# Performance work log

Measured on AMD Instinct MI355X. Metric: run time of the kernel, lower is better.

The kernel has to match this reference:

```python
import jax, jax.numpy as jnp
import numpy as np

NUM_HEADS = 8
LN_EPS = 1e-5

def _ln(x, g, b):
    mu = jnp.mean(x, axis=-1, keepdims=True)
    var = jnp.mean((x - mu) ** 2, axis=-1, keepdims=True)
    return (x - mu) * jax.lax.rsqrt(var + LN_EPS) * g + b

def _rel_index(H, W):
    coords = np.stack(np.meshgrid(np.arange(H), np.arange(W), indexing='ij'))  # (2,H,W)
    cf = coords.reshape(2, -1)
    rel = (cf[:, :, None] - cf[:, None, :]).transpose(1, 2, 0)  # (N,N,2)
    rel = rel + np.array([H - 1, W - 1])
    rel[..., 0] *= 2 * W - 1
    return rel.sum(-1)  # (N,N) int

def _biases(H, W):
    bh = np.arange(1 - H, H)
    bw = np.arange(1 - W, W)
    b = np.stack(np.meshgrid(bh, bw, indexing='ij')).reshape(2, -1).T
    return b.astype(np.float32)  # ((2H-1)*(2W-1), 2)

def setup_inputs() -> dict:
    key = jax.random.key(0)
    ks = jax.random.split(key, 8)
    dim, heads, pd = 256, NUM_HEADS, 16
    B, H, W = 256, 16, 16
    s = lambda k, shp, fan: jax.random.normal(k, shp, jnp.float32) * (fan ** -0.5)
    return {
        'x': jax.random.normal(ks[0], (B, dim, H, W), jnp.float32),
        'qkv_w': s(ks[1], (3 * dim, dim), dim), 'qkv_b': jnp.zeros((3 * dim,), jnp.float32),
        'proj_w': s(ks[2], (dim, dim), dim), 'proj_b': jnp.zeros((dim,), jnp.float32),
        'pos_proj_w': s(ks[3], (pd, 2), 2), 'pos_proj_b': jnp.zeros((pd,), jnp.float32),
        'ln1_g': jnp.ones((pd,), jnp.float32), 'ln1_b': jnp.zeros((pd,), jnp.float32),
        'fc1_w': s(ks[4], (pd, pd), pd), 'fc1_b': jnp.zeros((pd,), jnp.float32),
        'ln2_g': jnp.ones((pd,), jnp.float32), 'ln2_b': jnp.zeros((pd,), jnp.float32),
        'fc2_w': s(ks[5], (pd, pd), pd), 'fc2_b': jnp.zeros((pd,), jnp.float32),
        'ln3_g': jnp.ones((pd,), jnp.float32), 'ln3_b': jnp.zeros((pd,), jnp.float32),
        'fc3_w': s(ks[6], (heads, pd), pd), 'fc3_b': jnp.zeros((heads,), jnp.float32),
    }

def reference(x, qkv_w, qkv_b, proj_w, proj_b, pos_proj_w, pos_proj_b,
              ln1_g, ln1_b, fc1_w, fc1_b, ln2_g, ln2_b, fc2_w, fc2_b,
              ln3_g, ln3_b, fc3_w, fc3_b):
    B, C, H, W = x.shape
    N, h = H * W, NUM_HEADS
    d = C // h
    scale = d ** -0.5
    xt = x.reshape(B, C, N).transpose(0, 2, 1)  # (B,N,C)
    qkv = (jnp.einsum('bnc,oc->bno', xt, qkv_w) + qkv_b)
    qkv = qkv.reshape(B, N, 3, h, d).transpose(2, 0, 3, 1, 4)  # (3,B,h,N,d)
    q, k, v = qkv[0] * scale, qkv[1], qkv[2]
    attn = jnp.einsum('bhnd,bhmd->bhnm', q, k)  # (B,h,N,N)
    # dynamic position bias MLP over ((2H-1)(2W-1), 2) offsets
    biases = jnp.asarray(_biases(H, W))
    p = biases @ pos_proj_w.T + pos_proj_b
    p = jax.nn.relu(_ln(p, ln1_g, ln1_b)) @ fc1_w.T + fc1_b
    p = jax.nn.relu(_ln(p, ln2_g, ln2_b)) @ fc2_w.T + fc2_b
    p = jax.nn.relu(_ln(p, ln3_g, ln3_b)) @ fc3_w.T + fc3_b  # (L, h)
    idx = jnp.asarray(_rel_index(H, W))  # (N,N)
    rpb = p[idx].transpose(2, 0, 1)  # (h,N,N)
    attn = jax.nn.softmax(attn + rpb[None], axis=-1)
    out = jnp.einsum('bhnm,bhmd->bhnd', attn, v).transpose(0, 2, 1, 3).reshape(B, N, C)
    out = jnp.einsum('bnc,oc->bno', out, proj_w) + proj_b
    return out.transpose(0, 2, 1).reshape(B, C, H, W)
```

## Files before the change

kernel.cpp:

```cpp
#include <hip/hip_runtime.h>

typedef __bf16 bf16;
typedef __bf16 bf16x8 __attribute__((ext_vector_type(8)));
typedef __bf16 bf16x4 __attribute__((ext_vector_type(4)));
typedef float f32x4 __attribute__((ext_vector_type(4)));
typedef float f32x16 __attribute__((ext_vector_type(16)));
typedef unsigned int u32;
typedef unsigned int u32x2 __attribute__((ext_vector_type(2)));
typedef unsigned int u32x4 __attribute__((ext_vector_type(4)));

#define MFMA16(a, b, c) __builtin_amdgcn_mfma_f32_16x16x32_bf16(a, b, c, 0, 0, 0)
#define MFMA32(a, b, c) __builtin_amdgcn_mfma_f32_32x32x16_bf16(a, b, c, 0, 0, 0)

__device__ __forceinline__ u32 pack2(float a, float b) {
  unsigned short ua = __builtin_bit_cast(unsigned short, (bf16)a);
  unsigned short ub = __builtin_bit_cast(unsigned short, (bf16)b);
  return (u32)ua | ((u32)ub << 16);
}

__device__ __forceinline__ void lnrelu16(const float* in, float* out,
                                         const float* __restrict__ g,
                                         const float* __restrict__ b) {
  float mu = 0.f;
#pragma unroll
  for (int t = 0; t < 16; ++t) mu += in[t];
  mu *= 0.0625f;
  float var = 0.f;
#pragma unroll
  for (int t = 0; t < 16; ++t) { float d = in[t] - mu; var += d * d; }
  var *= 0.0625f;
  float inv = rsqrtf(var + 1e-5f);
#pragma unroll
  for (int t = 0; t < 16; ++t) {
    float v = (in[t] - mu) * inv * g[t] + b[t];
    out[t] = fmaxf(v, 0.f);
  }
}

__global__ __launch_bounds__(256) void k_prep(
    const float* __restrict__ qkvw, bf16* __restrict__ wqkv,
    const float* __restrict__ pjw, bf16* __restrict__ wpj,
    const float* __restrict__ ppw, const float* __restrict__ ppb,
    const float* __restrict__ g1, const float* __restrict__ b1,
    const float* __restrict__ f1w, const float* __restrict__ f1b,
    const float* __restrict__ g2, const float* __restrict__ b2,
    const float* __restrict__ f2w, const float* __restrict__ f2b,
    const float* __restrict__ g3, const float* __restrict__ b3,
    const float* __restrict__ f3w, const float* __restrict__ f3b,
    float* __restrict__ ptab) {
  const int blk = blockIdx.x;
  if (blk < 96) {
    int t = blk * 256 + threadIdx.x;
    int lane = t & 63, fk = t >> 6;
    int ot = fk >> 3, kc = fk & 7;
    int o = ot * 16 + (lane & 15), cb = kc * 32 + (lane >> 4) * 8;
    const float* src = qkvw + o * 256 + cb;
    bf16x8 v;
#pragma unroll
    for (int j = 0; j < 8; ++j) v[j] = (bf16)src[j];
    *(bf16x8*)(wqkv + (size_t)t * 8) = v;
  } else if (blk < 160) {
    int i = (blk - 96) * 256 + threadIdx.x;
    if (i < 16384) {
      float4 v = ((const float4*)pjw)[i];
      bf16x4 o;
      o[0] = (bf16)v.x; o[1] = (bf16)v.y; o[2] = (bf16)v.z; o[3] = (bf16)v.w;
      ((bf16x4*)wpj)[i] = o;
    }
  } else {
    int l = (blk - 160) * 256 + threadIdx.x;
    if (l >= 961) return;
    float dh = (float)(l / 31) - 15.f;
    float dw = (float)(l % 31) - 15.f;
    float p[16], a[16], y[16];
#pragma unroll
    for (int t = 0; t < 16; ++t)
      p[t] = dh * ppw[2 * t] + dw * ppw[2 * t + 1] + ppb[t];
    lnrelu16(p, a, g1, b1);
#pragma unroll
    for (int t = 0; t < 16; ++t) {
      float s = f1b[t];
#pragma unroll
      for (int u = 0; u < 16; ++u) s += a[u] * f1w[t * 16 + u];
      y[t] = s;
    }
    lnrelu16(y, a, g2, b2);
#pragma unroll
    for (int t = 0; t < 16; ++t) {
      float s = f2b[t];
#pragma unroll
      for (int u = 0; u < 16; ++u) s += a[u] * f2w[t * 16 + u];
      p[t] = s;
    }
    lnrelu16(p, a, g3, b3);
#pragma unroll
    for (int t = 0; t < 8; ++t) {
      float s = f3b[t];
#pragma unroll
      for (int u = 0; u < 16; ++u) s += a[u] * f3w[t * 16 + u];
      ptab[l * 8 + t] = s;
    }
  }
}

__global__ __launch_bounds__(256) void k_bias(const float* __restrict__ ptab,
                                              bf16* __restrict__ Bsw) {
  int idx = blockIdx.x * 256 + threadIdx.x;
  int lane = idx & 63, tg = idx >> 6;
  int h = tg >> 6, qt = (tg >> 3) & 7, kt2 = tg & 7;
  int l31 = lane & 31, hi2 = lane >> 5;
  int n = qt * 32 + l31;
  int i1 = n >> 4, j1 = n & 15;
  bf16x8 o0, o1;
#pragma unroll
  for (int reg = 0; reg < 16; ++reg) {
    int key = kt2 * 32 + (reg & 3) + 8 * (reg >> 2) + 4 * hi2;
    int i2 = key >> 4, j2 = key & 15;
    int li = (i1 - i2 + 15) * 31 + (j1 - j2 + 15);
    bf16 v = (bf16)ptab[li * 8 + h];
    if (reg < 8) o0[reg] = v; else o1[reg - 8] = v;
  }
  bf16* dst = Bsw + tg * 1024 + lane * 16;
  *(bf16x8*)dst = o0;
  *(bf16x8*)(dst + 8) = o1;
}

__global__ __launch_bounds__(256) void k_qkv(
    const float* __restrict__ x, const bf16* __restrict__ Wf,
    const float* __restrict__ qb, bf16* __restrict__ q, bf16* __restrict__ kk,
    bf16* __restrict__ vT) {
  __shared__ bf16 Xl[64 * 256];
  __shared__ bf16 Vb[4][16 * 36];
  const int b = blockIdx.x >> 2;
  const int n_base = (blockIdx.x & 3) * 64;
  const int tid = threadIdx.x;
  const int lane = tid & 63;
  const int wo = tid >> 6;
  const int l15 = lane & 15, l4 = lane >> 4;

  {
    const float* xb = x + b * 65536 + n_base;
    const int p = tid & 3;
    const int Q = tid >> 2;
    const int nq = (Q & 15) * 4;
    const int cg = Q >> 4;
#pragma unroll
    for (int it = 0; it < 16; ++it) {
      const int c0 = (cg + it * 4) * 4;
      float4 v = *(const float4*)(xb + (c0 + p) * 256 + nq);
      u32 u0 = pack2(v.x, v.y);
      u32 u1 = pack2(v.z, v.w);
      u32 su0 = __shfl_xor(u0, 1);
      u32 su1 = __shfl_xor(u1, 1);
      u32 w, z;
      if (p & 1) {
        w = (su0 >> 16) | (u0 & 0xffff0000u);
        z = (su1 >> 16) | (u1 & 0xffff0000u);
      } else {
        w = (u0 & 0xffffu) | (su0 << 16);
        z = (u1 & 0xffffu) | (su1 << 16);
      }
      u32 sw = __shfl_xor(w, 2);
      u32 sz = __shfl_xor(z, 2);
      u32x2 o2;
      o2[0] = (p & 2) ? sz : w;
      o2[1] = (p & 2) ? z : sw;
      const int n = nq + p;
      const int wb = (2 * c0) ^ ((n & 7) << 4);
      *(u32x2*)((char*)Xl + n * 512 + wb) = o2;
    }
  }
  __syncthreads();

  const f32x4 fz = {0.f, 0.f, 0.f, 0.f};
  bf16* lb = Vb[wo];
  for (int og = 0; og < 3; ++og) {
    const int ot0 = wo * 12 + og * 4;
    f32x4 acc[4][4];
#pragma unroll
    for (int nt = 0; nt < 4; ++nt)
#pragma unroll
      for (int oi = 0; oi < 4; ++oi) acc[nt][oi] = fz;
#pragma unroll
    for (int kc = 0; kc < 8; ++kc) {
      bf16x8 afr[4], bfr[4];
#pragma unroll
      for (int nt = 0; nt < 4; ++nt) {
        int nn = nt * 16 + l15;
        int wb = (kc * 64 + l4 * 16) ^ ((nn & 7) << 4);
        afr[nt] = *(const bf16x8*)((const char*)Xl + nn * 512 + wb);
      }
#pragma unroll
      for (int oi = 0; oi < 4; ++oi)
        bfr[oi] = *(const bf16x8*)(Wf + ((((ot0 + oi) * 8) + kc) * 64 + lane) * 8);
#pragma unroll
      for (int nt = 0; nt < 4; ++nt)
#pragma unroll
        for (int oi = 0; oi < 4; ++oi)
          acc[nt][oi] = MFMA16(afr[nt], bfr[oi], acc[nt][oi]);
    }
#pragma unroll
    for (int oi = 0; oi < 4; ++oi) {
      int ot = ot0 + oi;
      int o = ot * 16 + l15;
      float bias = qb[o];
      int seg = o >> 8;
      int h = (o >> 5) & 7;
      int d = o & 31;
      int base = (b * 8 + h) * 8192;
#pragma unroll
      for (int pr = 0; pr < 2; ++pr) {
        f32x4 acc0 = acc[2 * pr][oi], acc1 = acc[2 * pr + 1][oi];
        int n0p = n_base + pr * 32;
        if (seg == 0) {
          bf16* dq = q + base + d;
#pragma unroll
          for (int nt = 0; nt < 2; ++nt)
#pragma unroll
            for (int r = 0; r < 4; ++r) {
              int n = n0p + nt * 16 + l4 * 4 + r;
              float v = nt ? acc1[r] : acc0[r];
              dq[n * 32] = (bf16)((v + bias) * 0.17677669529663687f);
            }
        } else if (seg == 1) {
          bf16* dk = kk + base + d;
#pragma unroll
          for (int nt = 0; nt < 2; ++nt)
#pragma unroll
            for (int r = 0; r < 4; ++r) {
              int n = n0p + nt * 16 + l4 * 4 + r;
              float v = nt ? acc1[r] : acc0[r];
              dk[n * 32] = (bf16)(v + bias);
            }
        } else {
#pragma unroll
          for (int nt = 0; nt < 2; ++nt) {
            f32x4 a = nt ? acc1 : acc0;
            *(u32*)(lb + l15 * 36 + nt * 16 + l4 * 4) =
                pack2(a[0] + bias, a[1] + bias);
            *(u32*)(lb + l15 * 36 + nt * 16 + l4 * 4 + 2) =
                pack2(a[2] + bias, a[3] + bias);
          }
          asm volatile("s_waitcnt lgkmcnt(0)" ::: "memory");
          __builtin_amdgcn_sched_barrier(0);
          int dl = lane >> 2, chv = lane & 3;
          bf16x4 rv0 = *(bf16x4*)(lb + dl * 36 + chv * 8);
          bf16x4 rv1 = *(bf16x4*)(lb + dl * 36 + chv * 8 + 4);
          asm volatile("s_waitcnt lgkmcnt(0)" ::: "memory");
          __builtin_amdgcn_sched_barrier(0);
          int d2 = (ot & 1) * 16 + dl;
          bf16* dv2 = vT + base + d2 * 256 + n0p + chv * 8;
          *(bf16x4*)dv2 = rv0;
          *(bf16x4*)(dv2 + 4) = rv1;
        }
      }
    }
  }
}

__global__ __launch_bounds__(256, 4) void k_attn(
    const bf16* __restrict__ q, const bf16* __restrict__ kk,
    const bf16* __restrict__ vT, const bf16* __restrict__ Bsw,
    bf16* __restrict__ ao) {
  __shared__ bf16 Kl[256 * 36];
  __shared__ bf16 Ob[4][32 * 36];
  const int bh = blockIdx.x;
  const int b = bh >> 3, h = bh & 7;
  const int tid = threadIdx.x;
  const int lane = tid & 63, wave = tid >> 6;
  const int l31 = lane & 31, hi = lane >> 5;

  const bf16* Kg = kk + bh * 8192;
#pragma unroll
  for (int i = 0; i < 4; ++i) {
    int t = tid + i * 256;
    int n = t >> 2, dc = t & 3;
    *(bf16x8*)(Kl + n * 36 + dc * 8) = *(const bf16x8*)(Kg + n * 32 + dc * 8);
  }
  __syncthreads();

  const bf16* Vg = vT + bh * 8192;
  bf16* ob = Ob[wave];
  for (int qi = 0; qi < 2; ++qi) {
    const int qt = wave * 2 + qi, q0 = qt * 32;
    bf16x8 qf0 = *(const bf16x8*)(q + bh * 8192 + (q0 + l31) * 32 + hi * 8);
    bf16x8 qf1 = *(const bf16x8*)(q + bh * 8192 + (q0 + l31) * 32 + 16 + hi * 8);
    const bf16* bq = Bsw + (h * 8 + qt) * 8192 + lane * 16;
    float lsum = 0.f;
    f32x16 o;
#pragma unroll
    for (int i = 0; i < 16; ++i) o[i] = 0.f;
#pragma unroll
    for (int kt2 = 0; kt2 < 8; ++kt2) {
      u32x4 w0 = *(const u32x4*)(bq + kt2 * 1024);
      u32x4 w1 = *(const u32x4*)(bq + kt2 * 1024 + 8);
      f32x16 acc;
#pragma unroll
      for (int j = 0; j < 4; ++j) {
        acc[2 * j] = __builtin_bit_cast(float, w0[j] << 16);
        acc[2 * j + 1] = __builtin_bit_cast(float, w0[j] & 0xffff0000u);
        acc[8 + 2 * j] = __builtin_bit_cast(float, w1[j] << 16);
        acc[8 + 2 * j + 1] = __builtin_bit_cast(float, w1[j] & 0xffff0000u);
      }
      bf16x8 kf0 = *(const bf16x8*)(Kl + (kt2 * 32 + l31) * 36 + hi * 8);
      bf16x8 kf1 = *(const bf16x8*)(Kl + (kt2 * 32 + l31) * 36 + 16 + hi * 8);
      acc = MFMA32(kf0, qf0, acc);
      acc = MFMA32(kf1, qf1, acc);
      u32 lo[4], hw[4];
#pragma unroll
      for (int qq = 0; qq < 4; ++qq) {
        float e0 = __expf(acc[4 * qq]);
        float e1 = __expf(acc[4 * qq + 1]);
        float e2 = __expf(acc[4 * qq + 2]);
        float e3 = __expf(acc[4 * qq + 3]);
        lsum += (e0 + e1) + (e2 + e3);
        lo[qq] = pack2(e0, e1);
        hw[qq] = pack2(e2, e3);
      }
#pragma unroll
      for (int sb = 0; sb < 2; ++sb) {
        u32 keep_lo = hi ? lo[2 * sb + 1] : lo[2 * sb];
        u32 keep_hi = hi ? hw[2 * sb + 1] : hw[2 * sb];
        u32 send_lo = hi ? lo[2 * sb] : lo[2 * sb + 1];
        u32 send_hi = hi ? hw[2 * sb] : hw[2 * sb + 1];
        u32 rlo = __shfl_xor(send_lo, 32);
        u32 rhi = __shfl_xor(send_hi, 32);
        u32x4 bw;
        bw[0] = hi ? rlo : keep_lo;
        bw[1] = hi ? rhi : keep_hi;
        bw[2] = hi ? keep_lo : rlo;
        bw[3] = hi ? keep_hi : rhi;
        bf16x8 pf = __builtin_bit_cast(bf16x8, bw);
        bf16x8 vf = *(const bf16x8*)(Vg + l31 * 256 + kt2 * 32 + sb * 16 + hi * 8);
        o = MFMA32(vf, pf, o);
      }
    }
    lsum += __shfl_xor(lsum, 32);
    const float inv = 1.f / lsum;
#pragma unroll
    for (int qq = 0; qq < 4; ++qq) {
      *(u32*)(ob + l31 * 36 + 8 * qq + 4 * hi) =
          pack2(o[4 * qq] * inv, o[4 * qq + 1] * inv);
      *(u32*)(ob + l31 * 36 + 8 * qq + 4 * hi + 2) =
          pack2(o[4 * qq + 2] * inv, o[4 * qq + 3] * inv);
    }
    asm volatile("s_waitcnt lgkmcnt(0)" ::: "memory");
    __builtin_amdgcn_sched_barrier(0);
    int n2 = lane >> 1, ch = lane & 1;
    bf16x4 r0 = *(bf16x4*)(ob + n2 * 36 + ch * 16);
    bf16x4 r1 = *(bf16x4*)(ob + n2 * 36 + ch * 16 + 4);
    bf16x4 r2 = *(bf16x4*)(ob + n2 * 36 + ch * 16 + 8);
    bf16x4 r3 = *(bf16x4*)(ob + n2 * 36 + ch * 16 + 12);
    asm volatile("s_waitcnt lgkmcnt(0)" ::: "memory");
    __builtin_amdgcn_sched_barrier(0);
    bf16* dst = ao + (b * 256 + q0 + n2) * 256 + h * 32 + ch * 16;
    *(bf16x4*)dst = r0;
    *(bf16x4*)(dst + 4) = r1;
    *(bf16x4*)(dst + 8) = r2;
    *(bf16x4*)(dst + 12) = r3;
  }
}

__global__ __launch_bounds__(512) void k_proj(
    const bf16* __restrict__ ao, const bf16* __restrict__ Wp,
    const float* __restrict__ pb, float* __restrict__ out) {
  __shared__ bf16 Sl[2][16 * 264];
  const int b = blockIdx.x & 255;
  const int oh = blockIdx.x >> 8;
  const int tid = threadIdx.x;
  const int lane = tid & 63, wave = tid >> 6;
  const int l15 = lane & 15, l4 = lane >> 4;
  const int ot = oh * 8 + wave;
  bf16x8 af[8];
  const bf16* wr = Wp + (ot * 16 + l15) * 256 + l4 * 8;
#pragma unroll
  for (int kc = 0; kc < 8; ++kc) af[kc] = *(const bf16x8*)(wr + kc * 32);
  float bias[4];
#pragma unroll
  for (int r = 0; r < 4; ++r) bias[r] = pb[ot * 16 + l4 * 4 + r];
  const bf16* aob = ao + b * 65536;
  float* outb = out + b * 65536 + ot * 16 * 256;
  const int sr = tid >> 5, sc = (tid & 31) * 8;

  *(bf16x8*)(Sl[0] + sr * 264 + sc) = *(const bf16x8*)(aob + sr * 256 + sc);
  __syncthreads();

  const f32x4 fz = {0.f, 0.f, 0.f, 0.f};
  for (int nt = 0; nt < 16; ++nt) {
    const int cur = nt & 1;
    if (nt < 15)
      *(bf16x8*)(Sl[cur ^ 1] + sr * 264 + sc) =
          *(const bf16x8*)(aob + ((nt + 1) * 16 + sr) * 256 + sc);
    f32x4 acc = fz;
#pragma unroll
    for (int kc = 0; kc < 8; ++kc) {
      bf16x8 bfr = *(const bf16x8*)(Sl[cur] + l15 * 264 + kc * 32 + l4 * 8);
      acc = MFMA16(af[kc], bfr, acc);
    }
#pragma unroll
    for (int r = 0; r < 4; ++r)
      outb[(l4 * 4 + r) * 256 + nt * 16 + l15] = acc[r] + bias[r];
    __syncthreads();
  }
}

extern "C" void kernel_launch(void* const* d_in, const int* in_sizes, int n_in,
                              void* d_out, int out_size, void* d_ws, size_t ws_size,
                              hipStream_t stream) {
  const float* x    = (const float*)d_in[0];
  const float* qkvw = (const float*)d_in[1];
  const float* qkvb = (const float*)d_in[2];
  const float* pjw  = (const float*)d_in[3];
  const float* pjb  = (const float*)d_in[4];
  const float* ppw  = (const float*)d_in[5];
  const float* ppb  = (const float*)d_in[6];
  const float* g1 = (const float*)d_in[7];   const float* b1 = (const float*)d_in[8];
  const float* f1w = (const float*)d_in[9];  const float* f1b = (const float*)d_in[10];
  const float* g2 = (const float*)d_in[11];  const float* b2 = (const float*)d_in[12];
  const float* f2w = (const float*)d_in[13]; const float* f2b = (const float*)d_in[14];
  const float* g3 = (const float*)d_in[15];  const float* b3 = (const float*)d_in[16];
  const float* f3w = (const float*)d_in[17]; const float* f3b = (const float*)d_in[18];
  float* out = (float*)d_out;

  bf16* wsq  = (bf16*)d_ws;
  bf16* wsk  = wsq + 16777216;
  bf16* wsv  = wsk + 16777216;
  bf16* wsao = wsv + 16777216;
  float* ptab = (float*)(wsao + 16777216);
  bf16* wqkv = (bf16*)(ptab + 8192);
  bf16* wpj  = wqkv + 196608;
  bf16* bsw  = wpj + 65536;

  hipLaunchKernelGGL(k_prep, dim3(164), dim3(256), 0, stream, qkvw, wqkv, pjw,
                     wpj, ppw, ppb, g1, b1, f1w, f1b, g2, b2, f2w, f2b, g3, b3,
                     f3w, f3b, ptab);
  hipLaunchKernelGGL(k_bias, dim3(128), dim3(256), 0, stream, ptab, bsw);
  hipLaunchKernelGGL(k_qkv, dim3(1024), dim3(256), 0, stream, x, wqkv, qkvb,
                     wsq, wsk, wsv);
  hipLaunchKernelGGL(k_attn, dim3(2048), dim3(256), 0, stream, wsq, wsk, wsv,
                     bsw, wsao);
  hipLaunchKernelGGL(k_proj, dim3(512), dim3(512), 0, stream, wsao, wpj, pjb, out);
}
```

Baseline: 160.6 us.

## Fuse QKV projection into per-(batch, head) attention kernel via LDS

The separate QKV GEMM kernel and attention kernel are merged into one kernel. Each (batch, head) block projects its own q, k and v into LDS from a double-buffered bf16 staging of x, then runs the attention loop on that LDS data. The weight prep is reordered so each head's slice is contiguous. This removes the global write and re-read of the q, k and vT intermediates and one launch. In exchange, each batch's input x is re-read and re-converted once per head. The kernel also uses about 77 KB of LDS with a lower occupancy bound.

```diff
diff --git a/kernel.cpp b/kernel.cpp
--- a/kernel.cpp
+++ b/kernel.cpp
@@ -37,8 +37,38 @@
   }
 }
 
+__device__ __forceinline__ void stage_slice(const float* __restrict__ xb,
+                                            int kc, bf16* dst, int tid) {
+  const int p = tid & 3;
+  const int Q = tid >> 2;
+  const int n0 = Q * 4;
+#pragma unroll
+  for (int it = 0; it < 8; ++it) {
+    const int c0 = it * 4;
+    float4 v = *(const float4*)(xb + (kc * 32 + c0 + p) * 256 + n0);
+    u32 u0 = pack2(v.x, v.y);
+    u32 u1 = pack2(v.z, v.w);
+    u32 su0 = __shfl_xor(u0, 1);
+    u32 su1 = __shfl_xor(u1, 1);
+    u32 w, z;
+    if (p & 1) {
+      w = (su0 >> 16) | (u0 & 0xffff0000u);
+      z = (su1 >> 16) | (u1 & 0xffff0000u);
+    } else {
+      w = (u0 & 0xffffu) | (su0 << 16);
+      z = (u1 & 0xffffu) | (su1 << 16);
+    }
+    u32 sw = __shfl_xor(w, 2);
+    u32 sz = __shfl_xor(z, 2);
+    u32x2 o2;
+    o2[0] = (p & 2) ? sz : w;
+    o2[1] = (p & 2) ? z : sw;
+    *(u32x2*)((char*)dst + (n0 + p) * 80 + 2 * c0) = o2;
+  }
+}
+
 __global__ __launch_bounds__(256) void k_prep(
-    const float* __restrict__ qkvw, bf16* __restrict__ wqkv,
+    const float* __restrict__ qkvw, bf16* __restrict__ whf,
     const float* __restrict__ pjw, bf16* __restrict__ wpj,
     const float* __restrict__ ppw, const float* __restrict__ ppb,
     const float* __restrict__ g1, const float* __restrict__ b1,
@@ -52,13 +82,16 @@
   if (blk < 96) {
     int t = blk * 256 + threadIdx.x;
     int lane = t & 63, fk = t >> 6;
-    int ot = fk >> 3, kc = fk & 7;
-    int o = ot * 16 + (lane & 15), cb = kc * 32 + (lane >> 4) * 8;
+    int kc = fk & 7, ht = fk >> 3;
+    int h = ht / 6, tt = ht % 6;
+    int seg = tt >> 1, dh = tt & 1;
+    int o = seg * 256 + h * 32 + dh * 16 + (lane & 15);
+    int cb = kc * 32 + (lane >> 4) * 8;
     const float* src = qkvw + o * 256 + cb;
     bf16x8 v;
 #pragma unroll
     for (int j = 0; j < 8; ++j) v[j] = (bf16)src[j];
-    *(bf16x8*)(wqkv + (size_t)t * 8) = v;
+    *(bf16x8*)(whf + (size_t)t * 8) = v;
   } else if (blk < 160) {
     int i = (blk - 96) * 256 + threadIdx.x;
     if (i < 16384) {
@@ -125,166 +158,96 @@
   *(bf16x8*)(dst + 8) = o1;
 }
 
-__global__ __launch_bounds__(256) void k_qkv(
-    const float* __restrict__ x, const bf16* __restrict__ Wf,
-    const float* __restrict__ qb, bf16* __restrict__ q, bf16* __restrict__ kk,
-    bf16* __restrict__ vT) {
-  __shared__ bf16 Xl[64 * 256];
-  __shared__ bf16 Vb[4][16 * 36];
-  const int b = blockIdx.x >> 2;
-  const int n_base = (blockIdx.x & 3) * 64;
-  const int tid = threadIdx.x;
-  const int lane = tid & 63;
-  const int wo = tid >> 6;
-  const int l15 = lane & 15, l4 = lane >> 4;
-
-  {
-    const float* xb = x + b * 65536 + n_base;
-    const int p = tid & 3;
-    const int Q = tid >> 2;
-    const int nq = (Q & 15) * 4;
-    const int cg = Q >> 4;
-#pragma unroll
-    for (int it = 0; it < 16; ++it) {
-      const int c0 = (cg + it * 4) * 4;
-      float4 v = *(const float4*)(xb + (c0 + p) * 256 + nq);
-      u32 u0 = pack2(v.x, v.y);
-      u32 u1 = pack2(v.z, v.w);
-      u32 su0 = __shfl_xor(u0, 1);
-      u32 su1 = __shfl_xor(u1, 1);
-      u32 w, z;
-      if (p & 1) {
-        w = (su0 >> 16) | (u0 & 0xffff0000u);
-        z = (su1 >> 16) | (u1 & 0xffff0000u);
-      } else {
-        w = (u0 & 0xffffu) | (su0 << 16);
-        z = (u1 & 0xffffu) | (su1 << 16);
-      }
-      u32 sw = __shfl_xor(w, 2);
-      u32 sz = __shfl_xor(z, 2);
-      u32x2 o2;
-      o2[0] = (p & 2) ? sz : w;
-      o2[1] = (p & 2) ? z : sw;
-      const int n = nq + p;
-      const int wb = (2 * c0) ^ ((n & 7) << 4);
-      *(u32x2*)((char*)Xl + n * 512 + wb) = o2;
-    }
-  }
-  __syncthreads();
-
-  const f32x4 fz = {0.f, 0.f, 0.f, 0.f};
-  bf16* lb = Vb[wo];
-  for (int og = 0; og < 3; ++og) {
-    const int ot0 = wo * 12 + og * 4;
-    f32x4 acc[4][4];
-#pragma unroll
-    for (int nt = 0; nt < 4; ++nt)
-#pragma unroll
-      for (int oi = 0; oi < 4; ++oi) acc[nt][oi] = fz;
-#pragma unroll
-    for (int kc = 0; kc < 8; ++kc) {
-      bf16x8 afr[4], bfr[4];
-#pragma unroll
-      for (int nt = 0; nt < 4; ++nt) {
-        int nn = nt * 16 + l15;
-        int wb = (kc * 64 + l4 * 16) ^ ((nn & 7) << 4);
-        afr[nt] = *(const bf16x8*)((const char*)Xl + nn * 512 + wb);
-      }
-#pragma unroll
-      for (int oi = 0; oi < 4; ++oi)
-        bfr[oi] = *(const bf16x8*)(Wf + ((((ot0 + oi) * 8) + kc) * 64 + lane) * 8);
-#pragma unroll
-      for (int nt = 0; nt < 4; ++nt)
-#pragma unroll
-        for (int oi = 0; oi < 4; ++oi)
-          acc[nt][oi] = MFMA16(afr[nt], bfr[oi], acc[nt][oi]);
-    }
-#pragma unroll
-    for (int oi = 0; oi < 4; ++oi) {
-      int ot = ot0 + oi;
-      int o = ot * 16 + l15;
-      float bias = qb[o];
-      int seg = o >> 8;
-      int h = (o >> 5) & 7;
-      int d = o & 31;
-      int base = (b * 8 + h) * 8192;
-#pragma unroll
-      for (int pr = 0; pr < 2; ++pr) {
-        f32x4 acc0 = acc[2 * pr][oi], acc1 = acc[2 * pr + 1][oi];
-        int n0p = n_base + pr * 32;
-        if (seg == 0) {
-          bf16* dq = q + base + d;
-#pragma unroll
-          for (int nt = 0; nt < 2; ++nt)
-#pragma unroll
-            for (int r = 0; r < 4; ++r) {
-              int n = n0p + nt * 16 + l4 * 4 + r;
-              float v = nt ? acc1[r] : acc0[r];
-              dq[n * 32] = (bf16)((v + bias) * 0.17677669529663687f);
-            }
-        } else if (seg == 1) {
-          bf16* dk = kk + base + d;
-#pragma unroll
-          for (int nt = 0; nt < 2; ++nt)
-#pragma unroll
-            for (int r = 0; r < 4; ++r) {
-              int n = n0p + nt * 16 + l4 * 4 + r;
-              float v = nt ? acc1[r] : acc0[r];
-              dk[n * 32] = (bf16)(v + bias);
-            }
-        } else {
-#pragma unroll
-          for (int nt = 0; nt < 2; ++nt) {
-            f32x4 a = nt ? acc1 : acc0;
-            *(u32*)(lb + l15 * 36 + nt * 16 + l4 * 4) =
-                pack2(a[0] + bias, a[1] + bias);
-            *(u32*)(lb + l15 * 36 + nt * 16 + l4 * 4 + 2) =
-                pack2(a[2] + bias, a[3] + bias);
-          }
-          asm volatile("s_waitcnt lgkmcnt(0)" ::: "memory");
-          __builtin_amdgcn_sched_barrier(0);
-          int dl = lane >> 2, chv = lane & 3;
-          bf16x4 rv0 = *(bf16x4*)(lb + dl * 36 + chv * 8);
-          bf16x4 rv1 = *(bf16x4*)(lb + dl * 36 + chv * 8 + 4);
-          asm volatile("s_waitcnt lgkmcnt(0)" ::: "memory");
-          __builtin_amdgcn_sched_barrier(0);
-          int d2 = (ot & 1) * 16 + dl;
-          bf16* dv2 = vT + base + d2 * 256 + n0p + chv * 8;
-          *(bf16x4*)dv2 = rv0;
-          *(bf16x4*)(dv2 + 4) = rv1;
-        }
-      }
-    }
-  }
-}
-
-__global__ __launch_bounds__(256, 4) void k_attn(
-    const bf16* __restrict__ q, const bf16* __restrict__ kk,
-    const bf16* __restrict__ vT, const bf16* __restrict__ Bsw,
+__global__ __launch_bounds__(256, 2) void k_fused(
+    const float* __restrict__ x, const bf16* __restrict__ Whf,
+    const float* __restrict__ qb, const bf16* __restrict__ Bsw,
     bf16* __restrict__ ao) {
-  __shared__ bf16 Kl[256 * 36];
-  __shared__ bf16 Ob[4][32 * 36];
-  const int bh = blockIdx.x;
-  const int b = bh >> 3, h = bh & 7;
+  __shared__ bf16 lds[38400];
+  bf16* Xs0 = lds;
+  bf16* Xs1 = lds + 10240;
+  bf16* qL  = lds;
+  bf16* kL  = lds + 20480;
+  bf16* vTL = lds + 29696;
+  const int b = blockIdx.x & 255;
+  const int h = blockIdx.x >> 8;
   const int tid = threadIdx.x;
   const int lane = tid & 63, wave = tid >> 6;
+  const int l15 = lane & 15, l4 = lane >> 4;
   const int l31 = lane & 31, hi = lane >> 5;
-
-  const bf16* Kg = kk + bh * 8192;
-#pragma unroll
-  for (int i = 0; i < 4; ++i) {
-    int t = tid + i * 256;
-    int n = t >> 2, dc = t & 3;
-    *(bf16x8*)(Kl + n * 36 + dc * 8) = *(const bf16x8*)(Kg + n * 32 + dc * 8);
-  }
+  const int w64 = wave * 64;
+  const float* xb = x + b * 65536;
+
+  const f32x4 fz = {0.f, 0.f, 0.f, 0.f};
+  f32x4 acc[4][6];
+#pragma unroll
+  for (int nt = 0; nt < 4; ++nt)
+#pragma unroll
+    for (int t = 0; t < 6; ++t) acc[nt][t] = fz;
+
+  stage_slice(xb, 0, Xs0, tid);
   __syncthreads();
-
-  const bf16* Vg = vT + bh * 8192;
-  bf16* ob = Ob[wave];
+#pragma unroll
+  for (int kc = 0; kc < 8; ++kc) {
+    if (kc < 7) stage_slice(xb, kc + 1, (kc & 1) ? Xs0 : Xs1, tid);
+    const bf16* Xc = (kc & 1) ? Xs1 : Xs0;
+    bf16x8 afr[4], bfr[6];
+#pragma unroll
+    for (int nt = 0; nt < 4; ++nt)
+      afr[nt] = *(const bf16x8*)((const char*)Xc + (w64 + nt * 16 + l15) * 80 +
+                                 l4 * 16);
+#pragma unroll
+    for (int t = 0; t < 6; ++t)
+      bfr[t] = *(const bf16x8*)(Whf + (((h * 6 + t) * 8 + kc) * 64 + lane) * 8);
+#pragma unroll
+    for (int nt = 0; nt < 4; ++nt)
+#pragma unroll
+      for (int t = 0; t < 6; ++t)
+        acc[nt][t] = MFMA16(afr[nt], bfr[t], acc[nt][t]);
+    __syncthreads();
+  }
+
+#pragma unroll
+  for (int t = 0; t < 2; ++t) {
+    float bias = qb[h * 32 + t * 16 + l15];
+    int d = t * 16 + l15;
+#pragma unroll
+    for (int nt = 0; nt < 4; ++nt)
+#pragma unroll
+      for (int r = 0; r < 4; ++r)
+        qL[(w64 + nt * 16 + l4 * 4 + r) * 36 + d] =
+            (bf16)((acc[nt][t][r] + bias) * 0.17677669529663687f);
+  }
+#pragma unroll
+  for (int t = 2; t < 4; ++t) {
+    float bias = qb[256 + h * 32 + (t - 2) * 16 + l15];
+    int d = (t - 2) * 16 + l15;
+#pragma unroll
+    for (int nt = 0; nt < 4; ++nt)
+#pragma unroll
+      for (int r = 0; r < 4; ++r)
+        kL[(w64 + nt * 16 + l4 * 4 + r) * 36 + d] = (bf16)(acc[nt][t][r] + bias);
+  }
+#pragma unroll
+  for (int t = 4; t < 6; ++t) {
+    float bias = qb[512 + h * 32 + (t - 4) * 16 + l15];
+    int d = (t - 4) * 16 + l15;
+#pragma unroll
+    for (int nt = 0; nt < 4; ++nt) {
+      int n0q = w64 + nt * 16 + l4 * 4;
+      u32x2 pk;
+      pk[0] = pack2(acc[nt][t][0] + bias, acc[nt][t][1] + bias);
+      pk[1] = pack2(acc[nt][t][2] + bias, acc[nt][t][3] + bias);
+      *(u32x2*)((char*)vTL + d * 544 + 2 * n0q) = pk;
+    }
+  }
+  __syncthreads();
+
+  bf16* ob = qL + w64 * 36;
   for (int qi = 0; qi < 2; ++qi) {
     const int qt = wave * 2 + qi, q0 = qt * 32;
-    bf16x8 qf0 = *(const bf16x8*)(q + bh * 8192 + (q0 + l31) * 32 + hi * 8);
-    bf16x8 qf1 = *(const bf16x8*)(q + bh * 8192 + (q0 + l31) * 32 + 16 + hi * 8);
+    bf16x8 qf0 = *(const bf16x8*)((const char*)qL + (q0 + l31) * 72 + hi * 16);
+    bf16x8 qf1 =
+        *(const bf16x8*)((const char*)qL + (q0 + l31) * 72 + 32 + hi * 16);
     const bf16* bq = Bsw + (h * 8 + qt) * 8192 + lane * 16;
     float lsum = 0.f;
     f32x16 o;
@@ -294,25 +257,27 @@
     for (int kt2 = 0; kt2 < 8; ++kt2) {
       u32x4 w0 = *(const u32x4*)(bq + kt2 * 1024);
       u32x4 w1 = *(const u32x4*)(bq + kt2 * 1024 + 8);
-      f32x16 acc;
+      f32x16 acs;
 #pragma unroll
       for (int j = 0; j < 4; ++j) {
-        acc[2 * j] = __builtin_bit_cast(float, w0[j] << 16);
-        acc[2 * j + 1] = __builtin_bit_cast(float, w0[j] & 0xffff0000u);
-        acc[8 + 2 * j] = __builtin_bit_cast(float, w1[j] << 16);
-        acc[8 + 2 * j + 1] = __builtin_bit_cast(float, w1[j] & 0xffff0000u);
+        acs[2 * j] = __builtin_bit_cast(float, w0[j] << 16);
+        acs[2 * j + 1] = __builtin_bit_cast(float, w0[j] & 0xffff0000u);
+        acs[8 + 2 * j] = __builtin_bit_cast(float, w1[j] << 16);
+        acs[8 + 2 * j + 1] = __builtin_bit_cast(float, w1[j] & 0xffff0000u);
       }
-      bf16x8 kf0 = *(const bf16x8*)(Kl + (kt2 * 32 + l31) * 36 + hi * 8);
-      bf16x8 kf1 = *(const bf16x8*)(Kl + (kt2 * 32 + l31) * 36 + 16 + hi * 8);
-      acc = MFMA32(kf0, qf0, acc);
-      acc = MFMA32(kf1, qf1, acc);
+      bf16x8 kf0 =
+          *(const bf16x8*)((const char*)kL + (kt2 * 32 + l31) * 72 + hi * 16);
+      bf16x8 kf1 = *(const bf16x8*)((const char*)kL + (kt2 * 32 + l31) * 72 +
+                                    32 + hi * 16);
+      acs = MFMA32(kf0, qf0, acs);
+      acs = MFMA32(kf1, qf1, acs);
       u32 lo[4], hw[4];
 #pragma unroll
       for (int qq = 0; qq < 4; ++qq) {
-        float e0 = __expf(acc[4 * qq]);
-        float e1 = __expf(acc[4 * qq + 1]);
-        float e2 = __expf(acc[4 * qq + 2]);
-        float e3 = __expf(acc[4 * qq + 3]);
+        float e0 = __expf(acs[4 * qq]);
+        float e1 = __expf(acs[4 * qq + 1]);
+        float e2 = __expf(acs[4 * qq + 2]);
+        float e3 = __expf(acs[4 * qq + 3]);
         lsum += (e0 + e1) + (e2 + e3);
         lo[qq] = pack2(e0, e1);
         hw[qq] = pack2(e2, e3);
@@ -331,7 +296,8 @@
         bw[2] = hi ? keep_lo : rlo;
         bw[3] = hi ? keep_hi : rhi;
         bf16x8 pf = __builtin_bit_cast(bf16x8, bw);
-        bf16x8 vf = *(const bf16x8*)(Vg + l31 * 256 + kt2 * 32 + sb * 16 + hi * 8);
+        bf16x8 vf = *(const bf16x8*)((const char*)vTL + l31 * 544 +
+                                     (kt2 * 64 + sb * 32 + hi * 16));
         o = MFMA32(vf, pf, o);
       }
     }
@@ -423,21 +389,17 @@
   float* out = (float*)d_out;
 
   bf16* wsq  = (bf16*)d_ws;
-  bf16* wsk  = wsq + 16777216;
-  bf16* wsv  = wsk + 16777216;
-  bf16* wsao = wsv + 16777216;
+  bf16* wsao = wsq + 3 * 16777216;
   float* ptab = (float*)(wsao + 16777216);
-  bf16* wqkv = (bf16*)(ptab + 8192);
-  bf16* wpj  = wqkv + 196608;
+  bf16* whf  = (bf16*)(ptab + 8192);
+  bf16* wpj  = whf + 196608;
   bf16* bsw  = wpj + 65536;
 
-  hipLaunchKernelGGL(k_prep, dim3(164), dim3(256), 0, stream, qkvw, wqkv, pjw,
+  hipLaunchKernelGGL(k_prep, dim3(164), dim3(256), 0, stream, qkvw, whf, pjw,
                      wpj, ppw, ppb, g1, b1, f1w, f1b, g2, b2, f2w, f2b, g3, b3,
                      f3w, f3b, ptab);
   hipLaunchKernelGGL(k_bias, dim3(128), dim3(256), 0, stream, ptab, bsw);
-  hipLaunchKernelGGL(k_qkv, dim3(1024), dim3(256), 0, stream, x, wqkv, qkvb,
-                     wsq, wsk, wsv);
-  hipLaunchKernelGGL(k_attn, dim3(2048), dim3(256), 0, stream, wsq, wsk, wsv,
+  hipLaunchKernelGGL(k_fused, dim3(2048), dim3(256), 0, stream, x, whf, qkvb,
                      bsw, wsao);
   hipLaunchKernelGGL(k_proj, dim3(512), dim3(512), 0, stream, wsao, wpj, pjb, out);
 }
```

Result: slower. 199.9 us (+24.4%).
